# Performance work log

Hardware: AMD Instinct MI355X
Metric: run time of the kernel (lower is better)

Reference implementation:

```python
import jax, jax.numpy as jnp
import numpy as np
from jax import lax

BN_EPS = 1e-5
NORM_EPS = 1e-8


def _conv(x, w, b, stride, pad):
    y = lax.conv_general_dilated(x, w, (stride, stride), [(pad, pad), (pad, pad)],
                                 dimension_numbers=('NCHW', 'OIHW', 'NCHW'))
    return y + b[None, :, None, None]


def _bn(x, g, b, m, v):
    inv = g / jnp.sqrt(v + BN_EPS)
    return x * inv[None, :, None, None] + (b - m * inv)[None, :, None, None]


def _maxpool2(x):
    return lax.reduce_window(x, -jnp.inf, lax.max, (1, 1, 2, 2), (1, 1, 2, 2), 'VALID')


def setup_inputs() -> dict:
    key = jax.random.key(0)
    ks = jax.random.split(key, 16)
    d = {}
    d['x'] = jax.random.normal(ks[0], (64, 3, 512, 512), dtype=jnp.float32)
    d['conv1_w'] = jax.random.normal(ks[1], (32, 1, 5, 5), jnp.float32) * 0.1
    d['conv1_b'] = jnp.zeros((32,), jnp.float32)
    d['bn1_g'] = jnp.ones((32,), jnp.float32)
    d['bn1_b'] = jnp.zeros((32,), jnp.float32)
    d['bn1_m'] = jax.random.normal(ks[2], (32,), jnp.float32) * 0.1
    d['bn1_v'] = jax.random.uniform(ks[3], (32,), jnp.float32) + 0.5
    d['conv2_w'] = jax.random.normal(ks[4], (64, 32, 3, 3), jnp.float32) * 0.05
    d['conv2_b'] = jnp.zeros((64,), jnp.float32)
    d['bn2_g'] = jnp.ones((64,), jnp.float32)
    d['bn2_b'] = jnp.zeros((64,), jnp.float32)
    d['bn2_m'] = jax.random.normal(ks[5], (64,), jnp.float32) * 0.1
    d['bn2_v'] = jax.random.uniform(ks[6], (64,), jnp.float32) + 0.5
    d['conv3_w'] = jax.random.normal(ks[7], (128, 64, 3, 3), jnp.float32) * 0.04
    d['conv3_b'] = jnp.zeros((128,), jnp.float32)
    d['bn3_g'] = jnp.ones((128,), jnp.float32)
    d['bn3_b'] = jnp.zeros((128,), jnp.float32)
    d['bn3_m'] = jax.random.normal(ks[8], (128,), jnp.float32) * 0.1
    d['bn3_v'] = jax.random.uniform(ks[9], (128,), jnp.float32) + 0.5
    d['fc1_w'] = jax.random.normal(ks[10], (256, 128), jnp.float32) * 0.08
    d['fc1_b'] = jnp.zeros((256,), jnp.float32)
    d['fc2_w'] = jax.random.normal(ks[11], (128, 256), jnp.float32) * 0.06
    d['fc2_b'] = jnp.zeros((128,), jnp.float32)
    return d


def reference(x, conv1_w, conv1_b, bn1_g, bn1_b, bn1_m, bn1_v,
              conv2_w, conv2_b, bn2_g, bn2_b, bn2_m, bn2_v,
              conv3_w, conv3_b, bn3_g, bn3_b, bn3_m, bn3_v,
              fc1_w, fc1_b, fc2_w, fc2_b):
    # ---- batched FFT feature extraction (replaces per-sample numpy loop) ----
    gray = 0.299 * x[:, 0] + 0.587 * x[:, 1] + 0.114 * x[:, 2]      # (B,H,W)
    mag = jnp.abs(jnp.fft.fftshift(jnp.fft.fft2(gray), axes=(-2, -1)))
    logm = jnp.log1p(mag)
    mu = logm.mean(axis=(-2, -1), keepdims=True)
    sd = logm.std(axis=(-2, -1), keepdims=True)
    f = ((logm - mu) / (sd + NORM_EPS))[:, None]                     # (B,1,H,W)
    # ---- conv stack (BatchNorm in inference mode) ----
    h = jax.nn.relu(_bn(_conv(f, conv1_w, conv1_b, 2, 2), bn1_g, bn1_b, bn1_m, bn1_v))
    h = _maxpool2(h)
    h = jax.nn.relu(_bn(_conv(h, conv2_w, conv2_b, 2, 1), bn2_g, bn2_b, bn2_m, bn2_v))
    h = _maxpool2(h)
    h = jax.nn.relu(_bn(_conv(h, conv3_w, conv3_b, 2, 1), bn3_g, bn3_b, bn3_m, bn3_v))
    h = h.mean(axis=(-2, -1))                                        # AdaptiveAvgPool2d(1) -> (B,128)
    # ---- MLP (Dropout is identity in eval) ----
    h = jax.nn.relu(h @ fc1_w.T + fc1_b)
    return jax.nn.relu(h @ fc2_w.T + fc2_b)
```

## Files before the change

### kernel.cpp

```cpp
#include <hip/hip_runtime.h>
#include <math.h>

#define PI_F 3.14159265358979323846f
#define KS 258

typedef float f2 __attribute__((ext_vector_type(2)));

__device__ __forceinline__ void fft512(float* re, float* im,
                                       const float* twr, const float* twi, int u) {
#pragma unroll
  for (int s = 0; s < 8; s += 2) {
    __syncthreads();
    {
      int h  = 1 << s;
      int j  = u & (h - 1);
      int a  = ((u >> s) << (s + 2)) + j;
      int i0 = a, i1 = a + h, i2 = a + 2 * h, i3 = a + 3 * h;
      float e0r = re[i0], e0i = im[i0];
      float e1r = re[i1], e1i = im[i1];
      float e2r = re[i2], e2i = im[i2];
      float e3r = re[i3], e3i = im[i3];
      int tis = j << (8 - s);
      float wsr = twr[tis], wsi = twi[tis];
      float t1r = e1r * wsr - e1i * wsi, t1i = e1r * wsi + e1i * wsr;
      float t3r = e3r * wsr - e3i * wsi, t3i = e3r * wsi + e3i * wsr;
      float b0r = e0r + t1r, b0i = e0i + t1i;
      float b1r = e0r - t1r, b1i = e0i - t1i;
      float b2r = e2r + t3r, b2i = e2i + t3i;
      float b3r = e2r - t3r, b3i = e2i - t3i;
      int ti0 = j << (7 - s);
      int ti1 = (j + h) << (7 - s);
      float w0r = twr[ti0], w0i = twi[ti0];
      float w1r = twr[ti1], w1i = twi[ti1];
      float u2r = b2r * w0r - b2i * w0i, u2i = b2r * w0i + b2i * w0r;
      float u3r = b3r * w1r - b3i * w1i, u3i = b3r * w1i + b3i * w1r;
      re[i0] = b0r + u2r; im[i0] = b0i + u2i;
      re[i2] = b0r - u2r; im[i2] = b0i - u2i;
      re[i1] = b1r + u3r; im[i1] = b1i + u3i;
      re[i3] = b1r - u3r; im[i3] = b1i - u3i;
    }
  }
  __syncthreads();
  {
#pragma unroll
    for (int k = 0; k < 2; ++k) {
      int i1 = u + k * 128;
      int i2 = i1 + 256;
      float wr = twr[i1], wi = twi[i1];
      float ur = re[i1], ui = im[i1];
      float vr = re[i2], vi = im[i2];
      float tr = vr * wr - vi * wi;
      float tq = vr * wi + vi * wr;
      re[i1] = ur + tr; im[i1] = ui + tq;
      re[i2] = ur - tr; im[i2] = ui - tq;
    }
  }
  __syncthreads();
}

__device__ __forceinline__ void init_tw(float* twr, float* twi, int t) {
  float s, c;
  sincosf(-2.0f * PI_F * (float)t * (1.0f / 512.0f), &s, &c);
  twr[t] = c; twi[t] = s;
}

__global__ __launch_bounds__(256) void k_rowfft(const float* __restrict__ x,
                                                float2* __restrict__ G) {
  __shared__ float re[1024], im[1024], twr[256], twi[256];
  int t = threadIdx.x;
  int q = blockIdx.x;
  int b = blockIdx.y;
  int f = t >> 7, u = t & 127;
  int r0 = 4 * q;
  const float* xb = x + ((size_t)b * 3 * 512 + r0) * 512;
  const float* xr = xb + (2 * f) * 512;
  float* reb = re + 512 * f;
  float* imb = im + 512 * f;
#pragma unroll
  for (int j = 0; j < 4; ++j) {
    int p = u + 128 * j;
    float a = 0.299f * xr[p]        + 0.587f * xr[262144 + p]  + 0.114f * xr[524288 + p];
    float c = 0.299f * xr[512 + p]  + 0.587f * xr[262656 + p]  + 0.114f * xr[524800 + p];
    int rv = __brev((unsigned)p) >> 23;
    reb[rv] = a; imb[rv] = c;
  }
  init_tw(twr, twi, t);
  fft512(reb, imb, twr, twi, u);
  int r0p = r0 + 2 * f;
  float2* G0 = G + ((size_t)b * 512 + r0p) * KS;
  float2* G1 = G0 + KS;
  for (int k = u; k <= 256; k += 128) {
    int mk = (512 - k) & 511;
    float zr = reb[k], zi = imb[k];
    float mr = reb[mk], mi = imb[mk];
    G0[k] = make_float2(0.5f * (zr + mr), 0.5f * (zi - mi));
    G1[k] = make_float2(0.5f * (zi + mi), 0.5f * (mr - zr));
  }
}

__global__ __launch_bounds__(256) void k_transpose(const float2* __restrict__ G,
                                                   float2* __restrict__ GT) {
  __shared__ float2 ta[32][33];
  int kt = blockIdx.x, rt = blockIdx.y, b = blockIdx.z;
  int tx = threadIdx.x, ty = threadIdx.y;
  int k0 = kt * 32, r0 = rt * 32;
  const float2* Gb = G + (size_t)b * 512 * KS;
  float2* GTb = GT + (size_t)b * KS * 512;
#pragma unroll
  for (int i = 0; i < 32; i += 8) {
    int k = k0 + tx;
    float2 v = make_float2(0.0f, 0.0f);
    if (k < KS) v = Gb[(size_t)(r0 + ty + i) * KS + k];
    ta[ty + i][tx] = v;
  }
  __syncthreads();
#pragma unroll
  for (int i = 0; i < 32; i += 8) {
    int k = k0 + ty + i;
    if (k < KS) GTb[(size_t)k * 512 + r0 + tx] = ta[tx][ty + i];
  }
}

__global__ __launch_bounds__(256) void k_colfft(const float2* __restrict__ GT,
                                                float* __restrict__ S,
                                                double* __restrict__ stats) {
  __shared__ float re[1024], im[1024], twr[256], twi[256];
  __shared__ float ws1[4], ws2[4];
  int t  = threadIdx.x;
  int b  = blockIdx.y;
  int f = t >> 7, u = t & 127;
  int kc = 2 * blockIdx.x + f;
  bool valid = (kc <= 256);
  const float2* Gc = GT + ((size_t)b * KS + kc) * 512;
  float* reb = re + 512 * f;
  float* imb = im + 512 * f;
#pragma unroll
  for (int j = 0; j < 4; ++j) {
    int p = u + 128 * j;
    float2 v = Gc[p];
    int rv = __brev((unsigned)p) >> 23;
    reb[rv] = v.x; imb[rv] = v.y;
  }
  init_tw(twr, twi, t);
  fft512(reb, imb, twr, twi, u);
  int vrow = (kc + 256) & 511;
  bool mir = (kc >= 1) && (kc <= 255);
  float* Sb = S + (size_t)b * 262144;
  float s1 = 0.0f, s2 = 0.0f;
#pragma unroll
  for (int j = 0; j < 4; ++j) {
    int k = u + 128 * j;
    float mm = log1pf(sqrtf(reb[k] * reb[k] + imb[k] * imb[k]));
    if (valid) {
      Sb[(size_t)vrow * 512 + ((k + 256) & 511)] = mm;
      if (mir) Sb[(size_t)(256 - kc) * 512 + ((256 - k) & 511)] = mm;
      s1 += mm; s2 += mm * mm;
    }
  }
  float w = mir ? 2.0f : (valid ? 1.0f : 0.0f);
  s1 *= w; s2 *= w;
#pragma unroll
  for (int off = 32; off > 0; off >>= 1) {
    s1 += __shfl_down(s1, off);
    s2 += __shfl_down(s2, off);
  }
  int wvid = t >> 6;
  if ((t & 63) == 0) { ws1[wvid] = s1; ws2[wvid] = s2; }
  __syncthreads();
  if (t == 0) {
    float a = ws1[0] + ws1[1] + ws1[2] + ws1[3];
    float c = ws2[0] + ws2[1] + ws2[2] + ws2[3];
    atomicAdd(&stats[2 * b],     (double)a);
    atomicAdd(&stats[2 * b + 1], (double)c);
  }
}

__global__ void k_zero_stats(double* stats) {
  stats[threadIdx.x] = 0.0;
}

__global__ void k_stats(const double* __restrict__ stats, float2* __restrict__ muinv) {
  int i = threadIdx.x;
  double n  = 262144.0;
  double mu = stats[2 * i] / n;
  double va = stats[2 * i + 1] / n - mu * mu;
  if (va < 0.0) va = 0.0;
  double sd = sqrt(va);
  muinv[i] = make_float2((float)mu, (float)(1.0 / (sd + 1e-8)));
}

#define TS1 68
__global__ __launch_bounds__(256) void k_conv1(
    const float* __restrict__ S, const float2* __restrict__ muinv,
    const float* __restrict__ w, const float* __restrict__ cb,
    const float* __restrict__ g, const float* __restrict__ bb,
    const float* __restrict__ bm, const float* __restrict__ bv,
    float* __restrict__ h1) {
  __shared__ float tile[67 * TS1];
  int b = blockIdx.y;
  int by = blockIdx.x >> 3, bx = blockIdx.x & 7;
  int y0 = by * 16, x0 = bx * 16;
  int h0 = 4 * y0 - 2, w0 = 4 * x0 - 2;
  float2 mi = muinv[b];
  const float* Sb = S + (size_t)b * 262144;
  for (int idx = threadIdx.x; idx < 67 * 67; idx += 256) {
    int wl = idx / 67, hl = idx - wl * 67;
    int hh = h0 + hl, ww = w0 + wl;
    float val = 0.0f;
    if (hh >= 0 && hh < 512 && ww >= 0 && ww < 512)
      val = (Sb[(size_t)ww * 512 + hh] - mi.x) * mi.y;
    tile[wl * TS1 + hl] = val;
  }
  __syncthreads();
  int ty = threadIdx.x >> 4, tx = threadIdx.x & 15;
  float in[7][7];
#pragma unroll
  for (int j = 0; j < 7; ++j)
#pragma unroll
    for (int i = 0; i < 7; ++i)
      in[i][j] = tile[(4 * tx + j) * TS1 + 4 * ty + i];
  f2 P[7][5];
#pragma unroll
  for (int r = 0; r < 7; ++r)
#pragma unroll
    for (int c = 0; c < 5; ++c)
      P[r][c] = (f2){in[r][c], in[r][c + 2]};
  int Y = y0 + ty, X = x0 + tx;
  for (int oc = 0; oc < 32; ++oc) {
    const float* wo = w + oc * 25;
    f2 aA = (f2){0.0f, 0.0f};
    f2 aB = (f2){0.0f, 0.0f};
#pragma unroll
    for (int dy = 0; dy < 5; ++dy)
#pragma unroll
      for (int dx = 0; dx < 5; ++dx) {
        float wv = wo[dy * 5 + dx];
        f2 wv2 = (f2){wv, wv};
        aA = __builtin_elementwise_fma(wv2, P[dy][dx],     aA);
        aB = __builtin_elementwise_fma(wv2, P[dy + 2][dx], aB);
      }
    float m   = fmaxf(fmaxf(aA.x, aA.y), fmaxf(aB.x, aB.y));
    float inv = g[oc] / sqrtf(bv[oc] + 1e-5f);
    float sh  = cb[oc] * inv + bb[oc] - bm[oc] * inv;
    h1[(((size_t)b * 32 + oc) * 128 + Y) * 128 + X] = fmaxf(m * inv + sh, 0.0f);
  }
}

#define TS2 36
__global__ __launch_bounds__(512) void k_conv2(
    const float* __restrict__ h1, const float* __restrict__ w,
    const float* __restrict__ cb, const float* __restrict__ g,
    const float* __restrict__ bb, const float* __restrict__ bm,
    const float* __restrict__ bv, float* __restrict__ h2) {
  __shared__ __attribute__((aligned(16))) float tile[2][8 * 33 * TS2];
  int tid = threadIdx.x;
  int b = blockIdx.y;
  int rt = blockIdx.x >> 2, ct = blockIdx.x & 3;
  int ty0 = rt * 16, tx0 = ct * 16;
  int wv = tid >> 6;
  int lane = tid & 63;
  int qy = lane >> 3, qx = lane & 7;
  int iy0 = 2 * ty0 - 1, ix0 = 2 * tx0 - 1;
  int ocbase = wv * 8;
  f2 accA[8], accB[8];
#pragma unroll
  for (int q = 0; q < 8; ++q) {
    accA[q] = (f2){0.0f, 0.0f};
    accB[q] = (f2){0.0f, 0.0f};
  }

  int dsto[18], srco[18];
#pragma unroll
  for (int k = 0; k < 17; ++k) {
    int idx = tid + 512 * k;
    int ic = idx / 1089;
    int rem = idx - ic * 1089;
    int rr = rem / 33, cc = rem - rr * 33;
    int iy = iy0 + rr, ix = ix0 + cc;
    dsto[k] = (ic * 33 + rr) * TS2 + cc;
    srco[k] = (iy >= 0 && iy < 128 && ix >= 0 && ix < 128)
                  ? ((ic * 128 + iy) * 128 + ix) : -1;
  }
  {
    int idx = 8704 + tid;
    int ic = idx / 1089;
    int rem = idx - ic * 1089;
    int rr = rem / 33, cc = rem - rr * 33;
    int iy = iy0 + rr, ix = ix0 + cc;
    dsto[17] = (ic * 33 + rr) * TS2 + cc;
    srco[17] = (tid < 8 && iy >= 0 && iy < 128 && ix >= 0 && ix < 128)
                   ? ((ic * 128 + iy) * 128 + ix) : -1;
  }
  const float* h1b = h1 + (size_t)b * 32 * 16384;

  float rv[18];
#define C2_LOADR(ICT)                                                          \
  {                                                                            \
    _Pragma("unroll")                                                          \
    for (int k = 0; k < 18; ++k) {                                             \
      float v = 0.0f;                                                          \
      if (srco[k] >= 0) v = h1b[(ICT) * 131072 + srco[k]];                     \
      rv[k] = v;                                                               \
    }                                                                          \
  }

#define C2_WRITER(BUF)                                                         \
  {                                                                            \
    _Pragma("unroll")                                                          \
    for (int k = 0; k < 17; ++k) tile[BUF][dsto[k]] = rv[k];                   \
    if (tid < 8) tile[BUF][dsto[17]] = rv[17];                                 \
  }

  C2_LOADR(0);
  for (int ict = 0; ict < 4; ++ict) {
    int bs = ict & 1;
    C2_WRITER(bs);
    if (ict < 3) C2_LOADR(ict + 1);
    __syncthreads();
    const float* tb = tile[bs];
    int rbase = 4 * qy, cbase = 4 * qx;
#pragma unroll
    for (int ic = 0; ic < 8; ++ic) {
      f2 P[5][3];
#pragma unroll
      for (int i = 0; i < 5; ++i) {
        int base = (ic * 33 + rbase + i) * TS2 + cbase;
        float4 a = *reinterpret_cast<const float4*>(&tb[base]);
        float b4 = tb[base + 4];
        P[i][0] = (f2){a.x, a.z};
        P[i][1] = (f2){a.y, a.w};
        P[i][2] = (f2){a.z, b4};
      }
      const float* wic = w + ((size_t)ocbase * 32 + ict * 8 + ic) * 9;
#pragma unroll
      for (int q = 0; q < 8; ++q) {
        const float* wo = wic + (size_t)q * 32 * 9;
#pragma unroll
        for (int dy = 0; dy < 3; ++dy)
#pragma unroll
          for (int dx = 0; dx < 3; ++dx) {
            float wvv = wo[dy * 3 + dx];
            f2 wv2 = (f2){wvv, wvv};
            accA[q] = __builtin_elementwise_fma(wv2, P[dy][dx],     accA[q]);
            accB[q] = __builtin_elementwise_fma(wv2, P[dy + 2][dx], accB[q]);
          }
      }
    }
  }
  int Yp = (ty0 >> 1) + qy, Xp = (tx0 >> 1) + qx;
#pragma unroll
  for (int q = 0; q < 8; ++q) {
    int oc = ocbase + q;
    float m   = fmaxf(fmaxf(accA[q].x, accA[q].y), fmaxf(accB[q].x, accB[q].y));
    float inv = g[oc] / sqrtf(bv[oc] + 1e-5f);
    float sh  = cb[oc] * inv + bb[oc] - bm[oc] * inv;
    h2[(((size_t)b * 64 + oc) * 32 + Yp) * 32 + Xp] = fmaxf(m * inv + sh, 0.0f);
  }
#undef C2_LOADR
#undef C2_WRITER
}

#define TS3 34
__global__ __launch_bounds__(256) void k_conv3(
    const float* __restrict__ h2, const float* __restrict__ w,
    const float* __restrict__ cb, const float* __restrict__ g,
    const float* __restrict__ bb, const float* __restrict__ bm,
    const float* __restrict__ bv, float* __restrict__ gap) {
  __shared__ __attribute__((aligned(16))) float tile[8 * 33 * TS3];
  __shared__ float ws3[8][4];
  int tid = threadIdx.x;
  int ocg = blockIdx.x, b = blockIdx.y;
  int cy = tid >> 4, cx = tid & 15;
  f2 accP[4];
#pragma unroll
  for (int qp = 0; qp < 4; ++qp) accP[qp] = (f2){0.0f, 0.0f};

  for (int ict = 0; ict < 8; ++ict) {
    __syncthreads();
    for (int idx = tid; idx < 8 * 33 * 33; idx += 256) {
      int ic = idx / 1089;
      int rem = idx - ic * 1089;
      int rr = rem / 33, cc = rem - rr * 33;
      int iy = rr - 1, ix = cc - 1;
      float v = 0.0f;
      int icg = ict * 8 + ic;
      if (iy >= 0 && iy < 32 && ix >= 0 && ix < 32)
        v = h2[(((size_t)b * 64 + icg) * 32 + iy) * 32 + ix];
      tile[(ic * 33 + rr) * TS3 + cc] = v;
    }
    __syncthreads();
#pragma unroll
    for (int ic = 0; ic < 8; ++ic) {
      int icg = ict * 8 + ic;
      float in[3][3];
#pragma unroll
      for (int i = 0; i < 3; ++i) {
        const float2* r2 = reinterpret_cast<const float2*>(&tile[(ic * 33 + 2 * cy + i) * TS3 + 2 * cx]);
        float2 a = r2[0];
        in[i][0] = a.x; in[i][1] = a.y;
        in[i][2] = tile[(ic * 33 + 2 * cy + i) * TS3 + 2 * cx + 2];
      }
      const float* wic = w + ((size_t)(ocg * 8) * 64 + icg) * 9;
#pragma unroll
      for (int qp = 0; qp < 4; ++qp) {
        const float* wo0 = wic + (size_t)(2 * qp) * 64 * 9;
        const float* wo1 = wo0 + 64 * 9;
#pragma unroll
        for (int i = 0; i < 3; ++i)
#pragma unroll
          for (int j = 0; j < 3; ++j) {
            f2 wp = (f2){wo0[i * 3 + j], wo1[i * 3 + j]};
            f2 iv = (f2){in[i][j], in[i][j]};
            accP[qp] = __builtin_elementwise_fma(wp, iv, accP[qp]);
          }
      }
    }
  }
  int wvid = tid >> 6;
#pragma unroll
  for (int q = 0; q < 8; ++q) {
    int oc = ocg * 8 + q;
    float a = (q & 1) ? accP[q >> 1].y : accP[q >> 1].x;
    float inv = g[oc] / sqrtf(bv[oc] + 1e-5f);
    float sh  = cb[oc] * inv + bb[oc] - bm[oc] * inv;
    float v = fmaxf(a * inv + sh, 0.0f);
#pragma unroll
    for (int off = 32; off > 0; off >>= 1) v += __shfl_down(v, off);
    if ((tid & 63) == 0) ws3[q][wvid] = v;
  }
  __syncthreads();
  if (tid < 8)
    gap[(size_t)b * 128 + ocg * 8 + tid] =
        (ws3[tid][0] + ws3[tid][1] + ws3[tid][2] + ws3[tid][3]) * (1.0f / 256.0f);
}

__global__ __launch_bounds__(256) void k_fc(
    const float* __restrict__ gap,
    const float* __restrict__ w1, const float* __restrict__ b1,
    const float* __restrict__ w2, const float* __restrict__ b2,
    float* __restrict__ out) {
  __shared__ float gv[128], hv[256];
  int b = blockIdx.x, t = threadIdx.x;
  if (t < 128) gv[t] = gap[(size_t)b * 128 + t];
  __syncthreads();
  float a1 = b1[t];
  const float* wr = w1 + (size_t)t * 128;
  for (int k = 0; k < 128; ++k) a1 = fmaf(wr[k], gv[k], a1);
  hv[t] = fmaxf(a1, 0.0f);
  __syncthreads();
  if (t < 128) {
    float a2 = b2[t];
    const float* wr2 = w2 + (size_t)t * 256;
    for (int k = 0; k < 256; ++k) a2 = fmaf(wr2[k], hv[k], a2);
    out[(size_t)b * 128 + t] = fmaxf(a2, 0.0f);
  }
}

extern "C" void kernel_launch(void* const* d_in, const int* in_sizes, int n_in,
                              void* d_out, int out_size, void* d_ws, size_t ws_size,
                              hipStream_t stream) {
  (void)in_sizes; (void)n_in; (void)out_size; (void)ws_size;
  const float* x   = (const float*)d_in[0];
  const float* c1w = (const float*)d_in[1];
  const float* c1b = (const float*)d_in[2];
  const float* b1g = (const float*)d_in[3];
  const float* b1b = (const float*)d_in[4];
  const float* b1m = (const float*)d_in[5];
  const float* b1v = (const float*)d_in[6];
  const float* c2w = (const float*)d_in[7];
  const float* c2b = (const float*)d_in[8];
  const float* b2g = (const float*)d_in[9];
  const float* b2b = (const float*)d_in[10];
  const float* b2m = (const float*)d_in[11];
  const float* b2v = (const float*)d_in[12];
  const float* c3w = (const float*)d_in[13];
  const float* c3b = (const float*)d_in[14];
  const float* b3g = (const float*)d_in[15];
  const float* b3b = (const float*)d_in[16];
  const float* b3m = (const float*)d_in[17];
  const float* b3v = (const float*)d_in[18];
  const float* f1w = (const float*)d_in[19];
  const float* f1b = (const float*)d_in[20];
  const float* f2w = (const float*)d_in[21];
  const float* f2b = (const float*)d_in[22];
  float* out = (float*)d_out;

  char* ws = (char*)d_ws;
  float2* G     = (float2*)(ws + 0);
  float2* GT    = (float2*)(ws + 67633152ull);
  float*  S     = (float*) (ws + 135266304ull);
  double* stats = (double*)(ws + 202375168ull);
  float2* muinv = (float2*)(ws + 202376192ull);
  float*  gap   = (float*) (ws + 202376704ull);
  float*  h1    = (float*) (ws + 0);
  float*  h2    = (float*) (ws + 135266304ull);

  k_zero_stats<<<1, 128, 0, stream>>>(stats);
  k_rowfft   <<<dim3(128, 64), 256, 0, stream>>>(x, G);
  k_transpose<<<dim3(9, 16, 64), dim3(32, 8), 0, stream>>>(G, GT);
  k_colfft   <<<dim3(129, 64), 256, 0, stream>>>(GT, S, stats);
  k_stats    <<<1, 64, 0, stream>>>(stats, muinv);
  k_conv1    <<<dim3(64, 64), 256, 0, stream>>>(S, muinv, c1w, c1b, b1g, b1b, b1m, b1v, h1);
  k_conv2    <<<dim3(16, 64), 512, 0, stream>>>(h1, c2w, c2b, b2g, b2b, b2m, b2v, h2);
  k_conv3    <<<dim3(16, 64), 256, 0, stream>>>(h2, c3w, c3b, b3g, b3b, b3m, b3v, gap);
  k_fc       <<<64, 256, 0, stream>>>(gap, f1w, f1b, f2w, f2b, out);
}
```

Measured before the change: 902.4 us.

## Fuse transpose into column FFT via shared-memory staging; single-buffer conv2 tile

Removes the separate transpose kernel and its round trip through global memory. Each column-FFT block now loads an 8-column strip of the row-FFT output into padded shared memory and runs four pairs of 512-point FFTs from it, which cuts the block count to 33 per image. The strided 8-float2 reads from G may coalesce less well, and fewer, larger blocks lower parallelism. Conv2 separately drops its double-buffered tile in favour of a single buffer with an extra barrier per stage, trading load/compute overlap for less shared memory. Workspace offsets for h1 and h2 are reshuffled to match.

```diff
diff --git a/kernel.cpp b/kernel.cpp
--- a/kernel.cpp
+++ b/kernel.cpp
@@ -98,67 +98,59 @@
   }
 }
 
-__global__ __launch_bounds__(256) void k_transpose(const float2* __restrict__ G,
-                                                   float2* __restrict__ GT) {
-  __shared__ float2 ta[32][33];
-  int kt = blockIdx.x, rt = blockIdx.y, b = blockIdx.z;
-  int tx = threadIdx.x, ty = threadIdx.y;
-  int k0 = kt * 32, r0 = rt * 32;
-  const float2* Gb = G + (size_t)b * 512 * KS;
-  float2* GTb = GT + (size_t)b * KS * 512;
-#pragma unroll
-  for (int i = 0; i < 32; i += 8) {
-    int k = k0 + tx;
-    float2 v = make_float2(0.0f, 0.0f);
-    if (k < KS) v = Gb[(size_t)(r0 + ty + i) * KS + k];
-    ta[ty + i][tx] = v;
-  }
-  __syncthreads();
-#pragma unroll
-  for (int i = 0; i < 32; i += 8) {
-    int k = k0 + ty + i;
-    if (k < KS) GTb[(size_t)k * 512 + r0 + tx] = ta[tx][ty + i];
-  }
-}
-
-__global__ __launch_bounds__(256) void k_colfft(const float2* __restrict__ GT,
+__global__ __launch_bounds__(256) void k_colfft(const float2* __restrict__ G,
                                                 float* __restrict__ S,
                                                 double* __restrict__ stats) {
+  __shared__ float slr[512 * 9], sli[512 * 9];
   __shared__ float re[1024], im[1024], twr[256], twi[256];
   __shared__ float ws1[4], ws2[4];
-  int t  = threadIdx.x;
-  int b  = blockIdx.y;
+  int t = threadIdx.x;
+  int b = blockIdx.y;
+  int kc0 = blockIdx.x * 8;
+  const float2* Gb = G + (size_t)b * 512 * KS;
+#pragma unroll
+  for (int i = 0; i < 16; ++i) {
+    int idx = t + 256 * i;
+    int r = idx >> 3, c = idx & 7;
+    int kc = kc0 + c;
+    float2 v = make_float2(0.0f, 0.0f);
+    if (kc < KS) v = Gb[(size_t)r * KS + kc];
+    slr[r * 9 + c] = v.x;
+    sli[r * 9 + c] = v.y;
+  }
+  init_tw(twr, twi, t);
   int f = t >> 7, u = t & 127;
-  int kc = 2 * blockIdx.x + f;
-  bool valid = (kc <= 256);
-  const float2* Gc = GT + ((size_t)b * KS + kc) * 512;
   float* reb = re + 512 * f;
   float* imb = im + 512 * f;
-#pragma unroll
-  for (int j = 0; j < 4; ++j) {
-    int p = u + 128 * j;
-    float2 v = Gc[p];
-    int rv = __brev((unsigned)p) >> 23;
-    reb[rv] = v.x; imb[rv] = v.y;
-  }
-  init_tw(twr, twi, t);
-  fft512(reb, imb, twr, twi, u);
-  int vrow = (kc + 256) & 511;
-  bool mir = (kc >= 1) && (kc <= 255);
+  float s1 = 0.0f, s2 = 0.0f;
   float* Sb = S + (size_t)b * 262144;
-  float s1 = 0.0f, s2 = 0.0f;
-#pragma unroll
-  for (int j = 0; j < 4; ++j) {
-    int k = u + 128 * j;
-    float mm = log1pf(sqrtf(reb[k] * reb[k] + imb[k] * imb[k]));
-    if (valid) {
-      Sb[(size_t)vrow * 512 + ((k + 256) & 511)] = mm;
-      if (mir) Sb[(size_t)(256 - kc) * 512 + ((256 - k) & 511)] = mm;
-      s1 += mm; s2 += mm * mm;
-    }
-  }
-  float w = mir ? 2.0f : (valid ? 1.0f : 0.0f);
-  s1 *= w; s2 *= w;
+  for (int cp = 0; cp < 4; ++cp) {
+    int c = 2 * cp + f;
+    int kc = kc0 + c;
+    bool valid = (kc <= 256);
+    __syncthreads();
+#pragma unroll
+    for (int j = 0; j < 4; ++j) {
+      int p = u + 128 * j;
+      int rv = __brev((unsigned)p) >> 23;
+      reb[rv] = slr[p * 9 + c];
+      imb[rv] = sli[p * 9 + c];
+    }
+    fft512(reb, imb, twr, twi, u);
+    int vrow = (kc + 256) & 511;
+    bool mir = (kc >= 1) && (kc <= 255);
+    float wgt = mir ? 2.0f : 1.0f;
+#pragma unroll
+    for (int j = 0; j < 4; ++j) {
+      int k = u + 128 * j;
+      float mm = log1pf(sqrtf(reb[k] * reb[k] + imb[k] * imb[k]));
+      if (valid) {
+        Sb[(size_t)vrow * 512 + ((k + 256) & 511)] = mm;
+        if (mir) Sb[(size_t)(256 - kc) * 512 + ((256 - k) & 511)] = mm;
+        s1 += wgt * mm; s2 += wgt * mm * mm;
+      }
+    }
+  }
 #pragma unroll
   for (int off = 32; off > 0; off >>= 1) {
     s1 += __shfl_down(s1, off);
@@ -168,10 +160,8 @@
   if ((t & 63) == 0) { ws1[wvid] = s1; ws2[wvid] = s2; }
   __syncthreads();
   if (t == 0) {
-    float a = ws1[0] + ws1[1] + ws1[2] + ws1[3];
-    float c = ws2[0] + ws2[1] + ws2[2] + ws2[3];
-    atomicAdd(&stats[2 * b],     (double)a);
-    atomicAdd(&stats[2 * b + 1], (double)c);
+    atomicAdd(&stats[2 * b],     (double)(ws1[0] + ws1[1] + ws1[2] + ws1[3]));
+    atomicAdd(&stats[2 * b + 1], (double)(ws2[0] + ws2[1] + ws2[2] + ws2[3]));
   }
 }
 
@@ -252,7 +242,7 @@
     const float* __restrict__ cb, const float* __restrict__ g,
     const float* __restrict__ bb, const float* __restrict__ bm,
     const float* __restrict__ bv, float* __restrict__ h2) {
-  __shared__ __attribute__((aligned(16))) float tile[2][8 * 33 * TS2];
+  __shared__ __attribute__((aligned(16))) float tile[8 * 33 * TS2];
   int tid = threadIdx.x;
   int b = blockIdx.y;
   int rt = blockIdx.x >> 2, ct = blockIdx.x & 3;
@@ -304,20 +294,19 @@
     }                                                                          \
   }
 
-#define C2_WRITER(BUF)                                                         \
+#define C2_WRITER()                                                            \
   {                                                                            \
     _Pragma("unroll")                                                          \
-    for (int k = 0; k < 17; ++k) tile[BUF][dsto[k]] = rv[k];                   \
-    if (tid < 8) tile[BUF][dsto[17]] = rv[17];                                 \
+    for (int k = 0; k < 17; ++k) tile[dsto[k]] = rv[k];                        \
+    if (tid < 8) tile[dsto[17]] = rv[17];                                      \
   }
 
   C2_LOADR(0);
   for (int ict = 0; ict < 4; ++ict) {
-    int bs = ict & 1;
-    C2_WRITER(bs);
+    __syncthreads();
+    C2_WRITER();
+    __syncthreads();
     if (ict < 3) C2_LOADR(ict + 1);
-    __syncthreads();
-    const float* tb = tile[bs];
     int rbase = 4 * qy, cbase = 4 * qx;
 #pragma unroll
     for (int ic = 0; ic < 8; ++ic) {
@@ -325,8 +314,8 @@
 #pragma unroll
       for (int i = 0; i < 5; ++i) {
         int base = (ic * 33 + rbase + i) * TS2 + cbase;
-        float4 a = *reinterpret_cast<const float4*>(&tb[base]);
-        float b4 = tb[base + 4];
+        float4 a = *reinterpret_cast<const float4*>(&tile[base]);
+        float b4 = tile[base + 4];
         P[i][0] = (f2){a.x, a.z};
         P[i][1] = (f2){a.y, a.w};
         P[i][2] = (f2){a.z, b4};
@@ -487,18 +476,16 @@
 
   char* ws = (char*)d_ws;
   float2* G     = (float2*)(ws + 0);
-  float2* GT    = (float2*)(ws + 67633152ull);
   float*  S     = (float*) (ws + 135266304ull);
   double* stats = (double*)(ws + 202375168ull);
   float2* muinv = (float2*)(ws + 202376192ull);
   float*  gap   = (float*) (ws + 202376704ull);
-  float*  h1    = (float*) (ws + 0);
-  float*  h2    = (float*) (ws + 135266304ull);
+  float*  h1    = (float*) (ws + 67633152ull);
+  float*  h2    = (float*) (ws + 0);
 
   k_zero_stats<<<1, 128, 0, stream>>>(stats);
   k_rowfft   <<<dim3(128, 64), 256, 0, stream>>>(x, G);
-  k_transpose<<<dim3(9, 16, 64), dim3(32, 8), 0, stream>>>(G, GT);
-  k_colfft   <<<dim3(129, 64), 256, 0, stream>>>(GT, S, stats);
+  k_colfft   <<<dim3(33, 64), 256, 0, stream>>>(G, S, stats);
   k_stats    <<<1, 64, 0, stream>>>(stats, muinv);
   k_conv1    <<<dim3(64, 64), 256, 0, stream>>>(S, muinv, c1w, c1b, b1g, b1b, b1m, b1v, h1);
   k_conv2    <<<dim3(16, 64), 512, 0, stream>>>(h1, c2w, c2b, b2g, b2b, b2m, b2v, h2);
```

Measured after the change: 900.3 us. About the same (-0.2%).
